# Kernel optimization log

Measured on AMD Instinct MI355X. Metric: run time of the kernel, lower is better.

## Reference

```python
import jax, jax.numpy as jnp
import numpy as np
from jax import lax

D_MODEL, D_STATE, D_CONV, EXPAND = 64, 16, 4, 2
D_INNER = EXPAND * D_MODEL          # 128
DT_RANK = (D_MODEL + 15) // 16      # 4 = ceil(d_model/16), mamba_ssm 'auto'
B, L, N_IDX = 512, 256, 2048


def setup_inputs() -> dict:
    key = jax.random.key(0)
    ks = jax.random.split(key, 14)
    g = lambda k, shape, s: jax.random.normal(k, shape, jnp.float32) * s
    return {
        "reads": jax.random.normal(ks[0], (B, L, 4), jnp.float32),
        "sequenced_reads_indices": jax.random.randint(ks[1], (N_IDX,), 0, B),
        "exp_w": g(ks[2], (4, D_MODEL), 0.5),
        "exp_b": jnp.zeros((D_MODEL,), jnp.float32),
        "in_proj_w": g(ks[3], (D_MODEL, 2 * D_INNER), 0.1),
        "conv_w": g(ks[4], (D_INNER, 1, D_CONV), 0.3),
        "conv_b": jnp.zeros((D_INNER,), jnp.float32),
        "x_proj_w": g(ks[5], (D_INNER, DT_RANK + 2 * D_STATE), 0.1),
        "dt_w": g(ks[6], (DT_RANK, D_INNER), 0.3),
        "dt_b": jnp.full((D_INNER,), -4.6, jnp.float32),  # softplus(-4.6) ~ 0.01, mamba dt init scale
        "A_log": jnp.log(jnp.broadcast_to(jnp.arange(1, D_STATE + 1, dtype=jnp.float32), (D_INNER, D_STATE))),
        "D_skip": jnp.ones((D_INNER,), jnp.float32),
        "out_proj_w": g(ks[7], (D_INNER, D_MODEL), 0.1),
        "q_w": g(ks[8], (2 * D_MODEL, D_MODEL), 0.1),
        "q_b": jnp.zeros((D_MODEL,), jnp.float32),
        "k_w": g(ks[9], (2 * D_MODEL, D_MODEL), 0.1),
        "k_b": jnp.zeros((D_MODEL,), jnp.float32),
    }


def _mamba(x, in_proj_w, conv_w, conv_b, x_proj_w, dt_w, dt_b, A_log, D_skip, out_proj_w):
    # x: [b, l, d_model]
    xm, z = jnp.split(x @ in_proj_w, 2, axis=-1)  # each [b, l, d_inner]
    # causal depthwise conv over the sequence axis (pad left by d_conv-1, truncate to l)
    xc = lax.conv_general_dilated(
        xm.transpose(0, 2, 1), conv_w, (1,), [(D_CONV - 1, 0)],
        dimension_numbers=("NCH", "OIH", "NCH"), feature_group_count=D_INNER)
    xc = jax.nn.silu(xc + conv_b[None, :, None]).transpose(0, 2, 1)  # [b, l, d_inner]
    dt, Bm, Cm = jnp.split(xc @ x_proj_w, [DT_RANK, DT_RANK + D_STATE], axis=-1)
    delta = jax.nn.softplus(dt @ dt_w + dt_b)  # [b, l, d_inner]
    A = -jnp.exp(A_log)                        # [d_inner, d_state]

    def step(h, inp):
        d_t, B_t, C_t, u_t = inp  # [b,di], [b,ds], [b,ds], [b,di]
        h = jnp.exp(d_t[:, :, None] * A) * h + (d_t * u_t)[:, :, None] * B_t[:, None, :]
        return h, jnp.einsum("bdn,bn->bd", h, C_t)

    h0 = jnp.zeros((x.shape[0], D_INNER, D_STATE), x.dtype)
    xs = (delta.transpose(1, 0, 2), Bm.transpose(1, 0, 2),
          Cm.transpose(1, 0, 2), xc.transpose(1, 0, 2))
    _, ys = lax.scan(jax.checkpoint(step), h0, xs)  # ys: [l, b, d_inner]
    y = ys.transpose(1, 0, 2) + xc * D_skip
    return (y * jax.nn.silu(z)) @ out_proj_w  # [b, l, d_model]


def reference(reads, sequenced_reads_indices, exp_w, exp_b, in_proj_w, conv_w, conv_b,
              x_proj_w, dt_w, dt_b, A_log, D_skip, out_proj_w, q_w, q_b, k_w, k_b):
    x = reads @ exp_w + exp_b  # [b, l, d_model]
    enc = _mamba(x, in_proj_w, conv_w, conv_b, x_proj_w, dt_w, dt_b, A_log, D_skip, out_proj_w)
    mean_pooled = enc.mean(axis=1)        # [b, d_model]
    last_pooled = enc[:, -1, :]           # [b, d_model] (max pool computed in torch but unused)
    pooled = jnp.concatenate([mean_pooled, last_pooled], axis=-1)  # [b, 2*d_model]
    seq = pooled[sequenced_reads_indices]  # [n, 2*d_model]
    queries = seq @ q_w + q_b
    keys = pooled @ k_w + k_b
    return jnp.einsum("nd,md->nm", queries, keys)  # [n, b]
```

## Files before the change

kernel.cpp:

```cpp
#include <hip/hip_runtime.h>
#include <math.h>

#define L_SEQ 256
#define TILE 16
#define NSEG 16

typedef __attribute__((ext_vector_type(2))) float f32x2;
typedef __attribute__((ext_vector_type(4))) float f32x4;
typedef __attribute__((ext_vector_type(8))) _Float16 f16x8;
typedef __attribute__((ext_vector_type(2))) _Float16 f16x2;

__device__ __forceinline__ f32x2 fma2(f32x2 a, f32x2 b, f32x2 c) {
    return __builtin_elementwise_fma(a, b, c);
}
__device__ __forceinline__ f32x2 splat2(float x) { f32x2 v = {x, x}; return v; }
__device__ __forceinline__ float silu_f(float x) { return x / (1.f + __expf(-x)); }
__device__ __forceinline__ float sp2_f(float x) {
    return log2f(1.f + exp2f(x * 1.44269504f)) * 0.69314718f;
}

__global__ __launch_bounds__(256)
void k_prep(const float* __restrict__ exp_w, const float* __restrict__ exp_b,
            const float* __restrict__ in_proj_w, const float* __restrict__ x_proj_w,
            const float* __restrict__ dt_w,
            const float* __restrict__ conv_w, const float* __restrict__ conv_b,
            const float* __restrict__ A_log,
            _Float16* __restrict__ WT, _Float16* __restrict__ W2,
            float* __restrict__ bias2, int* __restrict__ sflag)
{
    const int t = threadIdx.x, blk = blockIdx.x;
    if (blk < 5) {
        const int base = blk * 4096;
        for (int i = base + t; i < base + 4096; i += 256) {
            const int row = i >> 7, k = i & 127;
            float v;
            if (row < 128) {
                v = x_proj_w[k * 36 + 0] * dt_w[row]
                  + x_proj_w[k * 36 + 1] * dt_w[128 + row]
                  + x_proj_w[k * 36 + 2] * dt_w[256 + row]
                  + x_proj_w[k * 36 + 3] * dt_w[384 + row];
            } else {
                v = x_proj_w[k * 36 + 4 + (row - 128)];
            }
            WT[i] = (_Float16)v;
        }
    } else if (blk == 5) {
        const int d = t & 127;
        const int col = (t < 128) ? d : (128 + d);
        float w0 = 0, w1 = 0, w2 = 0, w3 = 0, bb = 0;
        for (int k = 0; k < 64; ++k) {
            float w = in_proj_w[k * 256 + col];
            w0 = fmaf(exp_w[k], w, w0);
            w1 = fmaf(exp_w[64 + k], w, w1);
            w2 = fmaf(exp_w[128 + k], w, w2);
            w3 = fmaf(exp_w[192 + k], w, w3);
            bb = fmaf(exp_b[k], w, bb);
        }
        const float wx[4] = {w0, w1, w2, w3};
        if (t < 128) {
            for (int j = 0; j < 32; ++j) {
                float v = 0.f;
                if (j < 16)      v = conv_w[d * 4 + (j >> 2)] * wx[j & 3];
                else if (j < 20) v = conv_w[d * 4 + (j - 16)] * bb;
                W2[d * 32 + j] = (_Float16)v;
            }
            bias2[d] = conv_b[d];
        } else {
            for (int j = 0; j < 32; ++j) {
                float v = 0.f;
                if (j >= 12 && j < 16) v = wx[j - 12];
                else if (j == 19)      v = bb;
                W2[(128 + d) * 32 + j] = (_Float16)v;
            }
        }
    } else {
        __shared__ int ok;
        if (t == 0) ok = 1;
        __syncthreads();
        bool good = true;
        for (int i = t; i < 2048; i += 256) {
            float a = -__expf(A_log[i]);
            good = good && (fabsf(a + (float)((i & 15) + 1)) < 1e-3f);
        }
        if (!good) atomicAnd(&ok, 0);
        __syncthreads();
        if (t == 0) sflag[0] = ok;
    }
}

__global__ __launch_bounds__(256, 6)
void mamba_seg(const float* __restrict__ reads,
               const _Float16* __restrict__ WT, const _Float16* __restrict__ W2,
               const float* __restrict__ bias2, const float* __restrict__ dt_b,
               const float* __restrict__ A_log, const float* __restrict__ D_skip,
               const int* __restrict__ sflag,
               f16x2* __restrict__ Qg, f16x2* __restrict__ Pg, f16x2* __restrict__ Kg,
               float* __restrict__ GS, float* __restrict__ CZ, float* __restrict__ SL,
               int Bn)
{
    const int bx = blockIdx.x;
    const int b = bx >> 4, sidx = bx & 15;
    const int l_off = sidx * TILE;
    const int t = threadIdx.x;
    const int dd = t >> 1, g = t & 1;

    __shared__ __align__(16) _Float16 F[TILE * 40];
    __shared__ __align__(16) _Float16 XC[TILE * 136];
    __shared__ __align__(16) float    BC[TILE * 32];
    __shared__ _Float16               ZS[TILE * 128];
    __shared__ _Float16               DE[TILE * 128];

    const float dskip = D_skip[dd];
    const bool structured = (sflag[0] != 0);

    for (int i = t; i < TILE * 40; i += 256) {
        const int l = i / 40, j = i - l * 40;
        _Float16 v = (_Float16)0.f;
        if (j < 16) {
            const int row = l_off + l - 3 + (j >> 2);
            if (row >= 0) v = (_Float16)reads[((size_t)b * L_SEQ + row) * 4 + (j & 3)];
        } else if (j < 20) {
            v = (l_off + l - 3 + (j - 16) >= 0) ? (_Float16)1.f : (_Float16)0.f;
        }
        F[i] = v;
    }
    __syncthreads();

    const int lane = t & 63, wv = t >> 6;
    const int fcol = lane & 15, kq = lane >> 4, rbase = kq * 4;

#pragma unroll
    for (int i = 0; i < 4; ++i) {
        const int n = wv + 4 * i;
        f16x8 af = *(const f16x8*)&F[fcol * 40 + kq * 8];
        f16x8 bf = *(const f16x8*)&W2[(n * 16 + fcol) * 32 + kq * 8];
        f32x4 acc = {0.f, 0.f, 0.f, 0.f};
        acc = __builtin_amdgcn_mfma_f32_16x16x32_f16(af, bf, acc, 0, 0, 0);
        if (n < 8) {
            const int ch = n * 16 + fcol;
            const float bv = bias2[ch];
#pragma unroll
            for (int r = 0; r < 4; ++r)
                XC[(rbase + r) * 136 + ch] = (_Float16)silu_f(acc[r] + bv);
        } else {
            const int ch = (n - 8) * 16 + fcol;
#pragma unroll
            for (int r = 0; r < 4; ++r)
                ZS[(rbase + r) * 128 + ch] = (_Float16)silu_f(acc[r]);
        }
    }
    __syncthreads();

#pragma unroll
    for (int i = 0; i < 3; ++i) {
        const int n = wv + 4 * i;
        if (n < 10) {
            f32x4 acc = {0.f, 0.f, 0.f, 0.f};
#pragma unroll
            for (int ks = 0; ks < 4; ++ks) {
                const int ko = ks * 32 + kq * 8;
                f16x8 xa = *(const f16x8*)&XC[fcol * 136 + ko];
                f16x8 bf = *(const f16x8*)&WT[(n * 16 + fcol) * 128 + ko];
                acc = __builtin_amdgcn_mfma_f32_16x16x32_f16(xa, bf, acc, 0, 0, 0);
            }
            if (n < 8) {
                const int ch = n * 16 + fcol;
                const float db = dt_b[ch];
#pragma unroll
                for (int r = 0; r < 4; ++r)
                    DE[(rbase + r) * 128 + ch] = (_Float16)sp2_f(acc[r] + db);
            } else {
                const int jb = (n - 8) * 16 + fcol;
#pragma unroll
                for (int r = 0; r < 4; ++r)
                    BC[(rbase + r) * 32 + jb] = acc[r];
            }
        }
    }
    __syncthreads();

    f32x2 h2[4], P2[4], K2[4];
#pragma unroll
    for (int k = 0; k < 4; ++k) { h2[k] = splat2(0.f); P2[k] = splat2(1.f); K2[k] = splat2(0.f); }
    float gsum = 0.f;
    {
        auto scan_loop = [&](bool needpk) {
            for (int l = 0; l < TILE; ++l) {
                const float de = (float)DE[l * 128 + dd];
                const float zs = (float)ZS[l * 128 + dd];
                const float xc = (float)XC[l * 136 + dd];
                const float du = de * xc;
                f32x2 E2[4];
                if (structured) {
                    const float r  = exp2f(de * -1.44269504f);
                    const float r2 = r * r;
                    const float r4 = r2 * r2;
                    const float t1 = g ? (r4 * r4 * r) : r;
                    E2[0] = (f32x2){t1, t1 * r};
                    const f32x2 r2s = splat2(r2);
                    E2[1] = E2[0] * r2s;
                    E2[2] = E2[1] * r2s;
                    E2[3] = E2[2] * r2s;
                } else {
#pragma unroll
                    for (int k = 0; k < 4; ++k) {
                        float e0 = exp2f(de * (-__expf(A_log[dd * 16 + g * 8 + 2 * k])) * 1.44269504f);
                        float e1 = exp2f(de * (-__expf(A_log[dd * 16 + g * 8 + 2 * k + 1])) * 1.44269504f);
                        E2[k] = (f32x2){e0, e1};
                    }
                }
                const float4 Bq0 = *(const float4*)&BC[l * 32 + g * 8];
                const float4 Bq1 = *(const float4*)&BC[l * 32 + g * 8 + 4];
                const float4 Cq0 = *(const float4*)&BC[l * 32 + 16 + g * 8];
                const float4 Cq1 = *(const float4*)&BC[l * 32 + 16 + g * 8 + 4];
                const f32x2 B2[4] = {{Bq0.x, Bq0.y}, {Bq0.z, Bq0.w}, {Bq1.x, Bq1.y}, {Bq1.z, Bq1.w}};
                const f32x2 C2[4] = {{Cq0.x, Cq0.y}, {Cq0.z, Cq0.w}, {Cq1.x, Cq1.y}, {Cq1.z, Cq1.w}};
                const f32x2 dus = splat2(du), zss = splat2(zs);
                f32x2 yp2 = splat2(0.f);
#pragma unroll
                for (int k = 0; k < 4; ++k) {
                    h2[k] = fma2(E2[k], h2[k], dus * B2[k]);
                    yp2 = fma2(h2[k], C2[k], yp2);
                    if (needpk) {
                        P2[k] = P2[k] * E2[k];
                        K2[k] = fma2(zss, C2[k] * P2[k], K2[k]);
                    }
                }
                float yp = yp2.x + yp2.y;
                const float y = yp + __shfl_xor(yp, 1);
                gsum += fmaf(xc, dskip, y) * zs;
            }
        };
        if (sidx == 0) scan_loop(false);
        else           scan_loop(true);
    }

    {
        const size_t sb = (size_t)sidx * Bn + b;
#pragma unroll
        for (int k = 0; k < 4; ++k) {
            const size_t o = (sb * 8 + g * 4 + k) * 128 + dd;
            Qg[o] = (f16x2){(_Float16)h2[k].x, (_Float16)h2[k].y};
            if (sidx != 0) {
                Pg[o] = (f16x2){(_Float16)P2[k].x, (_Float16)P2[k].y};
                Kg[o] = (f16x2){(_Float16)K2[k].x, (_Float16)K2[k].y};
            }
        }
        if (g == 0) GS[sb * 128 + dd] = gsum;
        if (sidx == NSEG - 1) {
            const float zs_last = (float)ZS[(TILE - 1) * 128 + dd];
            const float xc_last = (float)XC[(TILE - 1) * 136 + dd];
#pragma unroll
            for (int k = 0; k < 8; ++k)
                CZ[((size_t)b * 16 + g * 8 + k) * 128 + dd] =
                    zs_last * BC[(TILE - 1) * 32 + 16 + g * 8 + k];
            if (g == 0) SL[(size_t)b * 128 + dd] = zs_last * xc_last * dskip;
        }
    }
}

template<int NS>
__global__ __launch_bounds__(128)
void stitch(const f16x2* __restrict__ Qg, const f16x2* __restrict__ Pg,
            const f16x2* __restrict__ Kg, const float* __restrict__ GS,
            const float* __restrict__ CZ, const float* __restrict__ SL,
            const float* __restrict__ out_proj_w,
            const float* __restrict__ k_w, const float* __restrict__ k_b,
            float* __restrict__ pooled, float* __restrict__ keysT, int Bn)
{
    const int b = blockIdx.x, d = threadIdx.x;
    __shared__ float gb[256];
    __shared__ float pl[128];

    float h[16];
    float gsum = GS[(size_t)b * 128 + d];
#pragma unroll
    for (int p = 0; p < 8; ++p) {
        f16x2 q = Qg[((size_t)b * 8 + p) * 128 + d];
        h[2 * p] = (float)q[0]; h[2 * p + 1] = (float)q[1];
    }
#pragma unroll
    for (int s = 1; s < NS; ++s) {
        const size_t sb = (size_t)s * Bn + b;
        gsum += GS[sb * 128 + d];
        float corr = 0.f;
#pragma unroll
        for (int p = 0; p < 8; ++p) {
            const size_t o = (sb * 8 + p) * 128 + d;
            f16x2 qv = Qg[o], pv = Pg[o], kv = Kg[o];
            corr = fmaf((float)kv[0], h[2 * p], corr);
            corr = fmaf((float)kv[1], h[2 * p + 1], corr);
            h[2 * p]     = fmaf((float)pv[0], h[2 * p],     (float)qv[0]);
            h[2 * p + 1] = fmaf((float)pv[1], h[2 * p + 1], (float)qv[1]);
        }
        gsum += corr;
    }
    float glast = SL[(size_t)b * 128 + d];
#pragma unroll
    for (int n = 0; n < 16; ++n)
        glast = fmaf(CZ[((size_t)b * 16 + n) * 128 + d], h[n], glast);

    gb[d] = gsum * (1.f / (float)L_SEQ);
    gb[128 + d] = glast;
    __syncthreads();
    {
        const int half = d >> 6, oc = d & 63;
        const float* gbp = &gb[half * 128];
        float s = 0.f;
#pragma unroll 16
        for (int i = 0; i < 128; ++i) s = fmaf(gbp[i], out_proj_w[i * 64 + oc], s);
        pooled[(size_t)b * 128 + d] = s;
        pl[d] = s;
    }
    __syncthreads();
    if (d < 64) {
        float s = k_b[d];
#pragma unroll 16
        for (int i = 0; i < 128; ++i) s = fmaf(pl[i], k_w[i * 64 + d], s);
        keysT[(size_t)d * Bn + b] = s;
    }
}

__global__ __launch_bounds__(128)
void qk_kernel(const float* __restrict__ pooled, const int* __restrict__ idx,
               const float* __restrict__ q_w, const float* __restrict__ q_b,
               const float* __restrict__ keysT, float* __restrict__ out, int B, int N)
{
    const int n0 = blockIdx.x * 2, t = threadIdx.x;
    const int n1 = n0 + 1;
    const bool has1 = (n1 < N);
    __shared__ float p0[128], p1[128];
    __shared__ float q0[64], q1[64];
    const int bi0 = idx[n0];
    const int bi1 = has1 ? idx[n1] : bi0;
    p0[t] = pooled[(size_t)bi0 * 128 + t];
    p1[t] = pooled[(size_t)bi1 * 128 + t];
    __syncthreads();
    if (t < 64) {
        float s = q_b[t];
#pragma unroll
        for (int i = 0; i < 128; ++i) s = fmaf(p0[i], q_w[i * 64 + t], s);
        q0[t] = s;
    } else {
        const int tt = t - 64;
        float s = q_b[tt];
#pragma unroll
        for (int i = 0; i < 128; ++i) s = fmaf(p1[i], q_w[i * 64 + tt], s);
        q1[tt] = s;
    }
    __syncthreads();
    for (int m0 = t * 4; m0 < B; m0 += 512) {
        f32x4 a0 = {0.f, 0.f, 0.f, 0.f}, a1 = {0.f, 0.f, 0.f, 0.f};
#pragma unroll 8
        for (int i = 0; i < 64; ++i) {
            const float4 kv = *(const float4*)&keysT[(size_t)i * B + m0];
            const float qa = q0[i], qb = q1[i];
            a0[0] = fmaf(qa, kv.x, a0[0]); a0[1] = fmaf(qa, kv.y, a0[1]);
            a0[2] = fmaf(qa, kv.z, a0[2]); a0[3] = fmaf(qa, kv.w, a0[3]);
            a1[0] = fmaf(qb, kv.x, a1[0]); a1[1] = fmaf(qb, kv.y, a1[1]);
            a1[2] = fmaf(qb, kv.z, a1[2]); a1[3] = fmaf(qb, kv.w, a1[3]);
        }
        *(f32x4*)&out[(size_t)n0 * B + m0] = a0;
        if (has1) *(f32x4*)&out[(size_t)n1 * B + m0] = a1;
    }
}


extern "C" void kernel_launch(void* const* d_in, const int* in_sizes, int n_in,
                              void* d_out, int out_size, void* d_ws, size_t ws_size,
                              hipStream_t stream)
{
    const float* reads      = (const float*)d_in[0];
    const int*   idx        = (const int*)d_in[1];
    const float* exp_w      = (const float*)d_in[2];
    const float* exp_b      = (const float*)d_in[3];
    const float* in_proj_w  = (const float*)d_in[4];
    const float* conv_w     = (const float*)d_in[5];
    const float* conv_b     = (const float*)d_in[6];
    const float* x_proj_w   = (const float*)d_in[7];
    const float* dt_w       = (const float*)d_in[8];
    const float* dt_b       = (const float*)d_in[9];
    const float* A_log      = (const float*)d_in[10];
    const float* D_skip     = (const float*)d_in[11];
    const float* out_proj_w = (const float*)d_in[12];
    const float* q_w        = (const float*)d_in[13];
    const float* q_b        = (const float*)d_in[14];
    const float* k_w        = (const float*)d_in[15];
    const float* k_b        = (const float*)d_in[16];

    const int B = in_sizes[0] / (L_SEQ * 4);
    const int N = in_sizes[1];

    char* wsb = (char*)d_ws;
    size_t off = 0;
    auto alloc = [&](size_t bytes) {
        size_t o = off;
        off = (off + bytes + 255) & ~(size_t)255;
        return o;
    };

    float*     pooled = (float*)(wsb + alloc((size_t)B * 128 * 4));
    float*     keysT  = (float*)(wsb + alloc((size_t)B * 64 * 4));
    _Float16*  WT     = (_Float16*)(wsb + alloc(160 * 128 * 2));
    _Float16*  W2     = (_Float16*)(wsb + alloc(256 * 32 * 2));
    float*     bias2  = (float*)(wsb + alloc(128 * 4));
    int*       sflag  = (int*)(wsb + alloc(256));

    const size_t pairs = (size_t)B * NSEG * 8 * 128;
    f16x2* Qg = (f16x2*)(wsb + alloc(pairs * 4));
    f16x2* Pg = (f16x2*)(wsb + alloc(pairs * 4));
    f16x2* Kg = (f16x2*)(wsb + alloc(pairs * 4));
    float* GS = (float*)(wsb + alloc((size_t)B * NSEG * 128 * 4));
    float* CZ = (float*)(wsb + alloc((size_t)B * 16 * 128 * 4));
    float* SL = (float*)(wsb + alloc((size_t)B * 128 * 4));

    k_prep<<<7, 256, 0, stream>>>(exp_w, exp_b, in_proj_w, x_proj_w, dt_w,
                                  conv_w, conv_b, A_log, WT, W2, bias2, sflag);
    mamba_seg<<<B * NSEG, 256, 0, stream>>>(reads, WT, W2, bias2, dt_b,
                                            A_log, D_skip, sflag, Qg, Pg, Kg,
                                            GS, CZ, SL, B);
    stitch<NSEG><<<B, 128, 0, stream>>>(Qg, Pg, Kg, GS, CZ, SL, out_proj_w, k_w, k_b,
                                        pooled, keysT, B);
    qk_kernel<<<(N + 1) / 2, 128, 0, stream>>>(pooled, idx, q_w, q_b, keysT,
                                               (float*)d_out, B, N);
}
```

Before: 130.5 us.

## Precompute decay ratio, interleave scan operands in LDS, split stitch across thread pairs

The softplus stage now also stores 1/(1+e^x), which equals exp(-delta), so the structured scan derives its decay powers without a per-step exp2. Delta, the ratio, silu(z) and xc are packed into one interleaved fp16x4 LDS array so each scan step does a single vector load. The y·z accumulation moves into a vector accumulator, and the cross-lane shuffle and D-skip term are applied once after the loop instead of every step. The stitch kernel runs 256 threads per batch row, splitting the state and the matvec reductions across thread pairs, which adds shuffles and a larger LDS footprint for the mamba_seg kernel.

```diff
diff --git a/kernel.cpp b/kernel.cpp
--- a/kernel.cpp
+++ b/kernel.cpp
@@ -8,16 +8,21 @@
 typedef __attribute__((ext_vector_type(2))) float f32x2;
 typedef __attribute__((ext_vector_type(4))) float f32x4;
 typedef __attribute__((ext_vector_type(8))) _Float16 f16x8;
+typedef __attribute__((ext_vector_type(4))) _Float16 f16x4;
 typedef __attribute__((ext_vector_type(2))) _Float16 f16x2;
 
 __device__ __forceinline__ f32x2 fma2(f32x2 a, f32x2 b, f32x2 c) {
     return __builtin_elementwise_fma(a, b, c);
 }
 __device__ __forceinline__ f32x2 splat2(float x) { f32x2 v = {x, x}; return v; }
-__device__ __forceinline__ float silu_f(float x) { return x / (1.f + __expf(-x)); }
-__device__ __forceinline__ float sp2_f(float x) {
-    return log2f(1.f + exp2f(x * 1.44269504f)) * 0.69314718f;
-}
+__device__ __forceinline__ float rcp_f(float x) {
+#if __has_builtin(__builtin_amdgcn_rcpf)
+    return __builtin_amdgcn_rcpf(x);
+#else
+    return 1.f / x;
+#endif
+}
+__device__ __forceinline__ float silu_f(float x) { return x * rcp_f(1.f + __expf(-x)); }
 
 __global__ __launch_bounds__(256)
 void k_prep(const float* __restrict__ exp_w, const float* __restrict__ exp_b,
@@ -106,9 +111,8 @@
 
     __shared__ __align__(16) _Float16 F[TILE * 40];
     __shared__ __align__(16) _Float16 XC[TILE * 136];
+    __shared__ __align__(8)  _Float16 DZR[TILE * 128 * 4];
     __shared__ __align__(16) float    BC[TILE * 32];
-    __shared__ _Float16               ZS[TILE * 128];
-    __shared__ _Float16               DE[TILE * 128];
 
     const float dskip = D_skip[dd];
     const bool structured = (sflag[0] != 0);
@@ -140,13 +144,16 @@
             const int ch = n * 16 + fcol;
             const float bv = bias2[ch];
 #pragma unroll
-            for (int r = 0; r < 4; ++r)
-                XC[(rbase + r) * 136 + ch] = (_Float16)silu_f(acc[r] + bv);
+            for (int r = 0; r < 4; ++r) {
+                const float hx = silu_f(acc[r] + bv);
+                XC[(rbase + r) * 136 + ch] = (_Float16)hx;
+                DZR[((rbase + r) * 128 + ch) * 4 + 3] = (_Float16)hx;
+            }
         } else {
             const int ch = (n - 8) * 16 + fcol;
 #pragma unroll
             for (int r = 0; r < 4; ++r)
-                ZS[(rbase + r) * 128 + ch] = (_Float16)silu_f(acc[r]);
+                DZR[((rbase + r) * 128 + ch) * 4 + 2] = (_Float16)silu_f(acc[r]);
         }
     }
     __syncthreads();
@@ -167,8 +174,16 @@
                 const int ch = n * 16 + fcol;
                 const float db = dt_b[ch];
 #pragma unroll
-                for (int r = 0; r < 4; ++r)
-                    DE[(rbase + r) * 128 + ch] = (_Float16)sp2_f(acc[r] + db);
+                for (int r = 0; r < 4; ++r) {
+                    const float dtr = fminf(acc[r] + db, 80.f);
+                    const float ex = __expf(dtr);
+                    const float opx = 1.f + ex;
+                    const float de = __logf(opx);
+                    const float rr = rcp_f(opx);
+                    const int o = ((rbase + r) * 128 + ch) * 4;
+                    DZR[o]     = (_Float16)de;
+                    DZR[o + 1] = (_Float16)rr;
+                }
             } else {
                 const int jb = (n - 8) * 16 + fcol;
 #pragma unroll
@@ -182,21 +197,23 @@
     f32x2 h2[4], P2[4], K2[4];
 #pragma unroll
     for (int k = 0; k < 4; ++k) { h2[k] = splat2(0.f); P2[k] = splat2(1.f); K2[k] = splat2(0.f); }
-    float gsum = 0.f;
+    f32x2 gs2 = splat2(0.f);
+    float xz = 0.f;
     {
         auto scan_loop = [&](bool needpk) {
             for (int l = 0; l < TILE; ++l) {
-                const float de = (float)DE[l * 128 + dd];
-                const float zs = (float)ZS[l * 128 + dd];
-                const float xc = (float)XC[l * 136 + dd];
+                const f16x4 dz = *(const f16x4*)&DZR[(l * 128 + dd) * 4];
+                const float de = (float)dz[0];
+                const float rr = (float)dz[1];
+                const float zs = (float)dz[2];
+                const float xc = (float)dz[3];
                 const float du = de * xc;
                 f32x2 E2[4];
                 if (structured) {
-                    const float r  = exp2f(de * -1.44269504f);
-                    const float r2 = r * r;
+                    const float r2 = rr * rr;
                     const float r4 = r2 * r2;
-                    const float t1 = g ? (r4 * r4 * r) : r;
-                    E2[0] = (f32x2){t1, t1 * r};
+                    const float t1 = g ? (r4 * r4 * rr) : rr;
+                    E2[0] = (f32x2){t1, t1 * rr};
                     const f32x2 r2s = splat2(r2);
                     E2[1] = E2[0] * r2s;
                     E2[2] = E2[1] * r2s;
@@ -226,9 +243,8 @@
                         K2[k] = fma2(zss, C2[k] * P2[k], K2[k]);
                     }
                 }
-                float yp = yp2.x + yp2.y;
-                const float y = yp + __shfl_xor(yp, 1);
-                gsum += fmaf(xc, dskip, y) * zs;
+                gs2 = fma2(yp2, zss, gs2);
+                xz = fmaf(xc, zs, xz);
             }
         };
         if (sidx == 0) scan_loop(false);
@@ -246,10 +262,14 @@
                 Kg[o] = (f16x2){(_Float16)K2[k].x, (_Float16)K2[k].y};
             }
         }
+        float gsp = gs2.x + gs2.y;
+        gsp += __shfl_xor(gsp, 1);
+        const float gsum = fmaf(dskip, xz, gsp);
         if (g == 0) GS[sb * 128 + dd] = gsum;
         if (sidx == NSEG - 1) {
-            const float zs_last = (float)ZS[(TILE - 1) * 128 + dd];
-            const float xc_last = (float)XC[(TILE - 1) * 136 + dd];
+            const f16x4 lastv = *(const f16x4*)&DZR[((TILE - 1) * 128 + dd) * 4];
+            const float zs_last = (float)lastv[2];
+            const float xc_last = (float)lastv[3];
 #pragma unroll
             for (int k = 0; k < 8; ++k)
                 CZ[((size_t)b * 16 + g * 8 + k) * 128 + dd] =
@@ -260,7 +280,7 @@
 }
 
 template<int NS>
-__global__ __launch_bounds__(128)
+__global__ __launch_bounds__(256)
 void stitch(const f16x2* __restrict__ Qg, const f16x2* __restrict__ Pg,
             const f16x2* __restrict__ Kg, const float* __restrict__ GS,
             const float* __restrict__ CZ, const float* __restrict__ SL,
@@ -268,56 +288,65 @@
             const float* __restrict__ k_w, const float* __restrict__ k_b,
             float* __restrict__ pooled, float* __restrict__ keysT, int Bn)
 {
-    const int b = blockIdx.x, d = threadIdx.x;
+    const int b = blockIdx.x, t = threadIdx.x;
+    const int d = t >> 1, g = t & 1;
     __shared__ float gb[256];
     __shared__ float pl[128];
 
-    float h[16];
-    float gsum = GS[(size_t)b * 128 + d];
-#pragma unroll
-    for (int p = 0; p < 8; ++p) {
-        f16x2 q = Qg[((size_t)b * 8 + p) * 128 + d];
-        h[2 * p] = (float)q[0]; h[2 * p + 1] = (float)q[1];
+    float h[8];
+    float gsum = (g == 0) ? GS[(size_t)b * 128 + d] : 0.f;
+#pragma unroll
+    for (int k = 0; k < 4; ++k) {
+        f16x2 q = Qg[((size_t)b * 8 + g * 4 + k) * 128 + d];
+        h[2 * k] = (float)q[0]; h[2 * k + 1] = (float)q[1];
     }
 #pragma unroll
     for (int s = 1; s < NS; ++s) {
         const size_t sb = (size_t)s * Bn + b;
-        gsum += GS[sb * 128 + d];
+        if (g == 0) gsum += GS[sb * 128 + d];
         float corr = 0.f;
 #pragma unroll
-        for (int p = 0; p < 8; ++p) {
-            const size_t o = (sb * 8 + p) * 128 + d;
+        for (int k = 0; k < 4; ++k) {
+            const size_t o = (sb * 8 + g * 4 + k) * 128 + d;
             f16x2 qv = Qg[o], pv = Pg[o], kv = Kg[o];
-            corr = fmaf((float)kv[0], h[2 * p], corr);
-            corr = fmaf((float)kv[1], h[2 * p + 1], corr);
-            h[2 * p]     = fmaf((float)pv[0], h[2 * p],     (float)qv[0]);
-            h[2 * p + 1] = fmaf((float)pv[1], h[2 * p + 1], (float)qv[1]);
+            corr = fmaf((float)kv[0], h[2 * k], corr);
+            corr = fmaf((float)kv[1], h[2 * k + 1], corr);
+            h[2 * k]     = fmaf((float)pv[0], h[2 * k],     (float)qv[0]);
+            h[2 * k + 1] = fmaf((float)pv[1], h[2 * k + 1], (float)qv[1]);
         }
         gsum += corr;
     }
-    float glast = SL[(size_t)b * 128 + d];
-#pragma unroll
-    for (int n = 0; n < 16; ++n)
-        glast = fmaf(CZ[((size_t)b * 16 + n) * 128 + d], h[n], glast);
-
-    gb[d] = gsum * (1.f / (float)L_SEQ);
-    gb[128 + d] = glast;
-    __syncthreads();
+    float glast = (g == 0) ? SL[(size_t)b * 128 + d] : 0.f;
+#pragma unroll
+    for (int k = 0; k < 8; ++k)
+        glast = fmaf(CZ[((size_t)b * 16 + g * 8 + k) * 128 + d], h[k], glast);
+
+    gsum += __shfl_xor(gsum, 1);
+    glast += __shfl_xor(glast, 1);
+    if (g == 0) { gb[d] = gsum * (1.f / (float)L_SEQ); gb[128 + d] = glast; }
+    __syncthreads();
+
     {
-        const int half = d >> 6, oc = d & 63;
+        const int oi = t >> 1;
+        const int half = oi >> 6, oc = oi & 63;
         const float* gbp = &gb[half * 128];
         float s = 0.f;
 #pragma unroll 16
-        for (int i = 0; i < 128; ++i) s = fmaf(gbp[i], out_proj_w[i * 64 + oc], s);
-        pooled[(size_t)b * 128 + d] = s;
-        pl[d] = s;
-    }
-    __syncthreads();
-    if (d < 64) {
-        float s = k_b[d];
+        for (int i = g * 64; i < g * 64 + 64; ++i)
+            s = fmaf(gbp[i], out_proj_w[i * 64 + oc], s);
+        s += __shfl_xor(s, 1);
+        if (g == 0) { pooled[(size_t)b * 128 + oi] = s; pl[oi] = s; }
+    }
+    __syncthreads();
+
+    if (t < 128) {
+        const int oc = t >> 1;
+        float s = (g == 0) ? k_b[oc] : 0.f;
 #pragma unroll 16
-        for (int i = 0; i < 128; ++i) s = fmaf(pl[i], k_w[i * 64 + d], s);
-        keysT[(size_t)d * Bn + b] = s;
+        for (int i = g * 64; i < g * 64 + 64; ++i)
+            s = fmaf(pl[i], k_w[i * 64 + oc], s);
+        s += __shfl_xor(s, 1);
+        if (g == 0) keysT[(size_t)oc * Bn + b] = s;
     }
 }
 
@@ -419,7 +448,7 @@
     mamba_seg<<<B * NSEG, 256, 0, stream>>>(reads, WT, W2, bias2, dt_b,
                                             A_log, D_skip, sflag, Qg, Pg, Kg,
                                             GS, CZ, SL, B);
-    stitch<NSEG><<<B, 128, 0, stream>>>(Qg, Pg, Kg, GS, CZ, SL, out_proj_w, k_w, k_b,
+    stitch<NSEG><<<B, 256, 0, stream>>>(Qg, Pg, Kg, GS, CZ, SL, out_proj_w, k_w, k_b,
                                         pooled, keysT, B);
     qk_kernel<<<(N + 1) / 2, 128, 0, stream>>>(pooled, idx, q_w, q_b, keysT,
                                                (float*)d_out, B, N);
```

Measured after the change: 127.3 us. -2.5%, faster.
